# Performance work log

Measured on AMD Instinct MI355X. Metric: run time of the kernel, lower is better.

The kernel has to match this reference:

```python
import jax, jax.numpy as jnp
import numpy as np

N, NFEAT, NHID, NCLASS, NHEADS = 4096, 512, 64, 40, 8
ALPHA = 0.2
NEG = -9e15


def setup_inputs() -> dict:
    key = jax.random.key(0)
    ks = jax.random.split(key, 6)
    x = jax.random.normal(ks[0], (N, NFEAT), dtype=jnp.float32)
    adj = jax.random.randint(ks[1], (2, N, N), 0, 2, dtype=jnp.int32)
    # Xavier-ish scaled params
    W1 = jax.random.normal(ks[2], (NHEADS, NFEAT, NHID), dtype=jnp.float32) * (1.0 / np.sqrt(NFEAT))
    a1 = jax.random.normal(ks[3], (NHEADS, 2, NHID), dtype=jnp.float32) * (1.0 / np.sqrt(2 * NHID))
    Wo = jax.random.normal(ks[4], (NHEADS * NHID, NCLASS), dtype=jnp.float32) * (1.0 / np.sqrt(NHEADS * NHID))
    ao = jax.random.normal(ks[5], (2, NCLASS), dtype=jnp.float32) * (1.0 / np.sqrt(2 * NCLASS))
    return {"x": x, "adj": adj, "W1": W1, "a1": a1, "Wo": Wo, "ao": ao}


def _gat_layer(h, adj_mask, W, a_src, a_dst, concat):
    # h: [N,F]; W: [...,F,F']; a_src/a_dst: [...,F']
    if W.ndim == 3:  # multi-head: [H,F,F']
        Wh = jnp.einsum('nf,hfd->hnd', h, W)              # [H,N,F']
        f1 = jnp.einsum('hnd,hd->hn', Wh, a_src)           # [H,N]
        f2 = jnp.einsum('hnd,hd->hn', Wh, a_dst)
        e = jax.nn.leaky_relu(f1[:, :, None] + f2[:, None, :], ALPHA)  # [H,N,N]
        e = jnp.where(adj_mask[None], e, NEG)
        att = jax.nn.softmax(e, axis=-1)
        out = jnp.einsum('hnm,hmd->hnd', att, Wh)          # [H,N,F']
    else:
        Wh = h @ W                                         # [N,F']
        f1 = Wh @ a_src
        f2 = Wh @ a_dst
        e = jax.nn.leaky_relu(f1[:, None] + f2[None, :], ALPHA)
        e = jnp.where(adj_mask, e, NEG)
        att = jax.nn.softmax(e, axis=-1)
        out = att @ Wh
    return jax.nn.elu(out) if concat else out


def reference(x, adj, W1, a1, Wo, ao):
    adj1 = adj[1] > 0
    adj0 = adj[0] > 0
    # layer 1: NHEADS heads, concat=True
    h = _gat_layer(x, adj1, W1, a1[:, 0], a1[:, 1], concat=True)   # [H,N,NHID]
    h = jnp.transpose(h, (1, 0, 2)).reshape(x.shape[0], -1)        # [N, H*NHID]
    # output layer: concat=False, then outer ELU + log_softmax
    out = _gat_layer(h, adj0, Wo, ao[0], ao[1], concat=False)      # [N, NCLASS]
    out = jax.nn.elu(out)
    return jax.nn.log_softmax(out, axis=1)
```

## Files before the change

### kernel.cpp

```cpp
#include <hip/hip_runtime.h>
#include <hip/hip_bf16.h>

#define N      4096
#define NFEAT  512
#define NHID   64
#define NHEADS 8
#define NCLASS 40
#define ALPHA  0.2f
#define LOG2E  1.44269504f

typedef unsigned short u16;
typedef unsigned int   u32;
typedef __attribute__((ext_vector_type(8))) short bf16x8;
typedef __attribute__((ext_vector_type(4))) float f32x4;

__device__ __forceinline__ float b2f(u16 u) {
    return __uint_as_float(((u32)u) << 16);
}
__device__ __forceinline__ u32 rnd_hi(float f) {
    u32 u = __float_as_uint(f);
    return u + 0x7FFFu + ((u >> 16) & 1u);
}
__device__ __forceinline__ u32 pk2(float lo, float hi) {
    __hip_bfloat162 h = __float22bfloat162_rn(make_float2(lo, hi));
    return *(u32*)&h;
}
__device__ __forceinline__ u16 f2b(float f) {
    return (u16)(rnd_hi(f) >> 16);
}
__device__ __forceinline__ float ex2(float t) {
    return __builtin_amdgcn_exp2f(t);
}
__device__ __forceinline__ bf16x8 ones_frag() {
    union { u16 u[8]; bf16x8 v; } o;
    #pragma unroll
    for (int j = 0; j < 8; ++j) o.u[j] = 0x3F80;
    return o.v;
}

__global__ __launch_bounds__(256) void kcx(const float* __restrict__ x,
                                           u16* __restrict__ xb) {
    const int g = blockIdx.x * 256 + threadIdx.x;
    const size_t base = (size_t)g * 8;
    float4 v0 = *(const float4*)&x[base];
    float4 v1 = *(const float4*)&x[base + 4];
    uint4 o;
    o.x = pk2(v0.x, v0.y); o.y = pk2(v0.z, v0.w);
    o.z = pk2(v1.x, v1.y); o.w = pk2(v1.z, v1.w);
    *(uint4*)&xb[base] = o;
}

__global__ __launch_bounds__(256) void kcw(const float* __restrict__ W1,
                                           u16* __restrict__ W1b) {
    __shared__ float ts[64 * 68];
    const int t  = threadIdx.x;
    const int f0 = blockIdx.x * 64;
    const int h  = blockIdx.y;
    #pragma unroll
    for (int i = 0; i < 4; ++i) {
        int flat = t + 256 * i;
        int row = flat >> 4;
        int c4  = (flat & 15) * 4;
        *(float4*)&ts[row * 68 + c4] =
            *(const float4*)&W1[((size_t)h * 512 + f0 + row) * 64 + c4];
    }
    __syncthreads();
    const int d  = t >> 2;
    const int fs = (t & 3) * 16;
    u32 p[8];
    #pragma unroll
    for (int j = 0; j < 8; ++j)
        p[j] = pk2(ts[(fs + 2 * j) * 68 + d], ts[(fs + 2 * j + 1) * 68 + d]);
    u32* dst = (u32*)&W1b[((size_t)(h * 64 + d)) * 512 + f0 + fs];
    *(uint4*)dst       = make_uint4(p[0], p[1], p[2], p[3]);
    *(uint4*)(dst + 4) = make_uint4(p[4], p[5], p[6], p[7]);
}

__global__ __launch_bounds__(256, 4) void k1m_gemm1(const u16* __restrict__ xb,
                                                    const u16* __restrict__ W1b,
                                                    const float* __restrict__ a1,
                                                    u16* __restrict__ Wh1T,
                                                    float* __restrict__ E1p,
                                                    float* __restrict__ E1n,
                                                    float* __restrict__ E2p,
                                                    float* __restrict__ E2n) {
    __shared__ u16 xs[64 * 72];
    __shared__ u16 wvs[64 * 72];
    const int t    = threadIdx.x;
    const int n0   = blockIdx.x * 64;
    const int h    = blockIdx.y;
    const int lane = t & 63;
    const int l15  = lane & 15;
    const int q    = lane >> 4;
    const int wrow = (t >> 6) * 16;
    f32x4 acc[4];
    #pragma unroll
    for (int df = 0; df < 4; ++df)
        #pragma unroll
        for (int r = 0; r < 4; ++r) acc[df][r] = 0.f;
    for (int f0 = 0; f0 < 512; f0 += 64) {
        uint4 sx[2], sw[2];
        #pragma unroll
        for (int i = 0; i < 2; ++i) {
            int flat = t + 256 * i;
            int row = flat >> 3;
            int c8  = (flat & 7) * 8;
            sx[i] = *(const uint4*)&xb[(size_t)(n0 + row) * 512 + f0 + c8];
            sw[i] = *(const uint4*)&W1b[((size_t)(h * 64 + row)) * 512 + f0 + c8];
        }
        __syncthreads();
        #pragma unroll
        for (int i = 0; i < 2; ++i) {
            int flat = t + 256 * i;
            int row = flat >> 3;
            int c8  = (flat & 7) * 8;
            *(uint4*)&xs[row * 72 + c8]  = sx[i];
            *(uint4*)&wvs[row * 72 + c8] = sw[i];
        }
        __syncthreads();
        #pragma unroll
        for (int ks = 0; ks < 2; ++ks) {
            int k0 = ks * 32 + q * 8;
            bf16x8 a = *(const bf16x8*)&xs[(wrow + l15) * 72 + k0];
            #pragma unroll
            for (int df = 0; df < 4; ++df) {
                bf16x8 b = *(const bf16x8*)&wvs[(df * 16 + l15) * 72 + k0];
                acc[df] = __builtin_amdgcn_mfma_f32_16x16x32_bf16(a, b, acc[df], 0, 0, 0);
            }
        }
    }
    #pragma unroll
    for (int df = 0; df < 4; ++df) {
        uint2 o;
        o.x = pk2(acc[df][0], acc[df][1]);
        o.y = pk2(acc[df][2], acc[df][3]);
        *(uint2*)&Wh1T[((size_t)(h * 64 + df * 16 + l15)) * 4096 + n0 + wrow + q * 4] = o;
    }
    float a1v[4], a2v[4];
    #pragma unroll
    for (int df = 0; df < 4; ++df) {
        a1v[df] = a1[h * 128 + df * 16 + l15];
        a2v[df] = a1[h * 128 + 64 + df * 16 + l15];
    }
    #pragma unroll
    for (int r = 0; r < 4; ++r) {
        float s1 = 0.f, s2 = 0.f;
        #pragma unroll
        for (int df = 0; df < 4; ++df) {
            s1 += acc[df][r] * a1v[df];
            s2 += acc[df][r] * a2v[df];
        }
        #pragma unroll
        for (int off = 8; off >= 1; off >>= 1) {
            s1 += __shfl_xor(s1, off);
            s2 += __shfl_xor(s2, off);
        }
        if (l15 == 0) {
            int n = n0 + wrow + q * 4 + r;
            float z1 = s1 * LOG2E, z2 = s2 * LOG2E;
            E1p[h * 4096 + n] = ex2(z1);
            E1n[h * 4096 + n] = ex2(ALPHA * z1);
            E2p[h * 4096 + n] = ex2(z2);
            E2n[h * 4096 + n] = ex2(ALPHA * z2);
        }
    }
}

__global__ __launch_bounds__(256, 4) void k3_attn1(const int* __restrict__ adj1,
                                                   const u16* __restrict__ Wh1T,
                                                   const float* __restrict__ E1p,
                                                   const float* __restrict__ E1n,
                                                   const float* __restrict__ E2p,
                                                   const float* __restrict__ E2n,
                                                   float* __restrict__ pacc1,
                                                   float* __restrict__ pz1) {
    __shared__ u16  wbf[64 * 136];
    __shared__ u16  whT[64 * 136];
    __shared__ float f1ps[64];
    __shared__ float f1ns[64];
    const int t     = threadIdx.x;
    const int n0    = blockIdx.x * 64;
    const int h     = blockIdx.y;
    const int chunk = blockIdx.z;
    const int lane  = t & 63;
    const int l15   = lane & 15;
    const int q     = lane >> 4;
    const int wrow  = (t >> 6) * 16;
    const int c4    = (t & 31) * 4;
    const int rg    = t >> 5;
    const bf16x8 bones = ones_frag();
    if (t < 64) {
        f1ps[t] = E1p[h * N + n0 + t];
        f1ns[t] = E1n[h * N + n0 + t];
    }
    f32x4 acc[5];
    #pragma unroll
    for (int df = 0; df < 5; ++df)
        #pragma unroll
        for (int r = 0; r < 4; ++r) acc[df][r] = 0.f;

    const int mbeg = chunk * 2048;
    int4 aprev[8];
    #pragma unroll
    for (int i = 0; i < 8; ++i)
        aprev[i] = *(const int4*)&adj1[(size_t)(n0 + rg + 8 * i) * N + mbeg + c4];
    float4 P2 = *(const float4*)&E2p[h * N + mbeg + c4];
    float4 N2 = *(const float4*)&E2n[h * N + mbeg + c4];
    __syncthreads();

    for (int m0 = mbeg; m0 < mbeg + 2048; m0 += 128) {
        #pragma unroll
        for (int i = 0; i < 8; ++i) {
            int rr = rg + 8 * i;
            int4 a4 = aprev[i];
            float cp = f1ps[rr];
            float cn = f1ns[rr];
            float w0 = a4.x ? fmaxf(cp * P2.x, cn * N2.x) : 0.f;
            float w1 = a4.y ? fmaxf(cp * P2.y, cn * N2.y) : 0.f;
            float w2 = a4.z ? fmaxf(cp * P2.z, cn * N2.z) : 0.f;
            float w3 = a4.w ? fmaxf(cp * P2.w, cn * N2.w) : 0.f;
            uint2 pk;
            pk.x = pk2(w0, w1);
            pk.y = pk2(w2, w3);
            *(uint2*)&wbf[rr * 136 + c4] = pk;
        }
        int mn = (m0 + 128 < mbeg + 2048) ? m0 + 128 : mbeg;
        #pragma unroll
        for (int i = 0; i < 8; ++i)
            aprev[i] = *(const int4*)&adj1[(size_t)(n0 + rg + 8 * i) * N + mn + c4];
        P2 = *(const float4*)&E2p[h * N + mn + c4];
        N2 = *(const float4*)&E2n[h * N + mn + c4];
        #pragma unroll
        for (int i = 0; i < 4; ++i) {
            int flat = t + 256 * i;
            int row = flat >> 4;
            int c8  = (flat & 15) * 8;
            *(uint4*)&whT[row * 136 + c8] =
                *(const uint4*)&Wh1T[((size_t)(h * 64 + row)) * 4096 + m0 + c8];
        }
        __syncthreads();
        #pragma unroll
        for (int ks = 0; ks < 4; ++ks) {
            int k0 = ks * 32 + q * 8;
            bf16x8 a = *(const bf16x8*)&wbf[(wrow + l15) * 136 + k0];
            #pragma unroll
            for (int df = 0; df < 4; ++df) {
                bf16x8 b = *(const bf16x8*)&whT[(df * 16 + l15) * 136 + k0];
                acc[df] = __builtin_amdgcn_mfma_f32_16x16x32_bf16(a, b, acc[df], 0, 0, 0);
            }
            acc[4] = __builtin_amdgcn_mfma_f32_16x16x32_bf16(a, bones, acc[4], 0, 0, 0);
        }
        __syncthreads();
    }
    const size_t rowbase = (size_t)(chunk * 8 + h) * 4096 + n0;
    #pragma unroll
    for (int r = 0; r < 4; ++r) {
        int nl = wrow + q * 4 + r;
        if (l15 == 0) pz1[rowbase + nl] = acc[4][r];
        #pragma unroll
        for (int df = 0; df < 4; ++df)
            pacc1[(rowbase + nl) * 64 + df * 16 + l15] = acc[df][r];
    }
}

__global__ __launch_bounds__(256) void k3b_norm(const float* __restrict__ pacc1,
                                                const float* __restrict__ pz1,
                                                float* __restrict__ h1) {
    const int g = blockIdx.x * 256 + threadIdx.x;
    const int d = g & 63;
    const int h = (g >> 6) & 7;
    const int n = g >> 9;
    const size_t i0 = (size_t)h * 4096 + n;
    float s = pacc1[i0 * 64 + d] + pacc1[(i0 + 8 * 4096) * 64 + d];
    float z = pz1[i0] + pz1[i0 + 8 * 4096];
    float v = s / fmaxf(z, 1e-30f);
    h1[(size_t)n * 512 + h * 64 + d] = v > 0.f ? v : __expf(v) - 1.f;
}

__global__ __launch_bounds__(256) void k4_gemm2(const float* __restrict__ h1,
                                                const float* __restrict__ Wo,
                                                const float* __restrict__ ao,
                                                float* __restrict__ E1op,
                                                float* __restrict__ E1on,
                                                float* __restrict__ E2op,
                                                float* __restrict__ E2on,
                                                u16* __restrict__ Wh2T) {
    const int t = threadIdx.x;
    const int c = t & 63;
    const int n = blockIdx.x * 4 + (t >> 6);
    float acc = 0.f;
    if (c < NCLASS) {
        const float* hrow = &h1[(size_t)n * 512];
        #pragma unroll 8
        for (int f = 0; f < 512; ++f)
            acc += hrow[f] * Wo[f * NCLASS + c];
        Wh2T[(size_t)c * 4096 + n] = f2b(acc);
    }
    float s1 = (c < NCLASS) ? acc * ao[c] : 0.f;
    float s2 = (c < NCLASS) ? acc * ao[NCLASS + c] : 0.f;
    #pragma unroll
    for (int off = 32; off >= 1; off >>= 1) {
        s1 += __shfl_xor(s1, off);
        s2 += __shfl_xor(s2, off);
    }
    if (c == 0) {
        float z1 = s1 * LOG2E, z2 = s2 * LOG2E;
        E1op[n] = ex2(z1);
        E1on[n] = ex2(ALPHA * z1);
        E2op[n] = ex2(z2);
        E2on[n] = ex2(ALPHA * z2);
    }
}

__global__ __launch_bounds__(256, 4) void k5a_attn2(const int* __restrict__ adj0,
                                                    const u16* __restrict__ Wh2T,
                                                    const float* __restrict__ E1op,
                                                    const float* __restrict__ E1on,
                                                    const float* __restrict__ E2op,
                                                    const float* __restrict__ E2on,
                                                    float* __restrict__ pacc,
                                                    float* __restrict__ pz) {
    __shared__ u16  wbf[64 * 136];
    __shared__ u16  whT[48 * 136];
    __shared__ float f1ps[64];
    __shared__ float f1ns[64];
    const int t     = threadIdx.x;
    const int n0    = blockIdx.x * 64;
    const int chunk = blockIdx.y;
    const int mbase = chunk * 256;
    const int lane  = t & 63;
    const int l15   = lane & 15;
    const int q     = lane >> 4;
    const int wrow  = (t >> 6) * 16;
    const int c4    = (t & 31) * 4;
    const int rg    = t >> 5;
    const bf16x8 bones = ones_frag();
    if (t < 64) {
        f1ps[t] = E1op[n0 + t];
        f1ns[t] = E1on[n0 + t];
    }
    #pragma unroll
    for (int i = 0; i < 5; ++i) {
        int idx = t + 256 * i;
        if (idx < 1088) whT[40 * 136 + idx] = 0;
    }
    f32x4 acc[4];
    #pragma unroll
    for (int df = 0; df < 4; ++df)
        #pragma unroll
        for (int r = 0; r < 4; ++r) acc[df][r] = 0.f;
    int4 aprev[8];
    #pragma unroll
    for (int i = 0; i < 8; ++i)
        aprev[i] = *(const int4*)&adj0[(size_t)(n0 + rg + 8 * i) * N + mbase + c4];
    float4 P2 = *(const float4*)&E2op[mbase + c4];
    float4 N2 = *(const float4*)&E2on[mbase + c4];
    __syncthreads();

    for (int mt = 0; mt < 2; ++mt) {
        int m0 = mbase + mt * 128;
        #pragma unroll
        for (int i = 0; i < 8; ++i) {
            int rr = rg + 8 * i;
            int4 a4 = aprev[i];
            float cp = f1ps[rr];
            float cn = f1ns[rr];
            float w0 = a4.x ? fmaxf(cp * P2.x, cn * N2.x) : 0.f;
            float w1 = a4.y ? fmaxf(cp * P2.y, cn * N2.y) : 0.f;
            float w2 = a4.z ? fmaxf(cp * P2.z, cn * N2.z) : 0.f;
            float w3 = a4.w ? fmaxf(cp * P2.w, cn * N2.w) : 0.f;
            uint2 pk;
            pk.x = pk2(w0, w1);
            pk.y = pk2(w2, w3);
            *(uint2*)&wbf[rr * 136 + c4] = pk;
        }
        int mn = mbase + ((mt + 1) & 1) * 128;
        #pragma unroll
        for (int i = 0; i < 8; ++i)
            aprev[i] = *(const int4*)&adj0[(size_t)(n0 + rg + 8 * i) * N + mn + c4];
        P2 = *(const float4*)&E2op[mn + c4];
        N2 = *(const float4*)&E2on[mn + c4];
        #pragma unroll
        for (int i = 0; i < 3; ++i) {
            int flat = t + 256 * i;
            if (flat < 640) {
                int row = flat >> 4;
                int c8  = (flat & 15) * 8;
                *(uint4*)&whT[row * 136 + c8] =
                    *(const uint4*)&Wh2T[(size_t)row * 4096 + m0 + c8];
            }
        }
        __syncthreads();
        #pragma unroll
        for (int ks = 0; ks < 4; ++ks) {
            int k0 = ks * 32 + q * 8;
            bf16x8 a = *(const bf16x8*)&wbf[(wrow + l15) * 136 + k0];
            #pragma unroll
            for (int df = 0; df < 3; ++df) {
                bf16x8 b = *(const bf16x8*)&whT[(df * 16 + l15) * 136 + k0];
                acc[df] = __builtin_amdgcn_mfma_f32_16x16x32_bf16(a, b, acc[df], 0, 0, 0);
            }
            acc[3] = __builtin_amdgcn_mfma_f32_16x16x32_bf16(a, bones, acc[3], 0, 0, 0);
        }
        __syncthreads();
    }
    #pragma unroll
    for (int r = 0; r < 4; ++r) {
        int n = n0 + wrow + q * 4 + r;
        if (l15 == 0) pz[(size_t)chunk * N + n] = acc[3][r];
        #pragma unroll
        for (int df = 0; df < 3; ++df) {
            int c = df * 16 + l15;
            if (c < NCLASS)
                pacc[((size_t)chunk * N + n) * NCLASS + c] = acc[df][r];
        }
    }
}

__global__ __launch_bounds__(256) void k5b_final(const float* __restrict__ pacc,
                                                 const float* __restrict__ pz,
                                                 float* __restrict__ out) {
    const int t = threadIdx.x;
    const int lane = t & 63;
    const int n = blockIdx.x * 4 + (t >> 6);
    float s = 0.f, Z = 0.f;
    #pragma unroll
    for (int ch = 0; ch < 16; ++ch) {
        Z += pz[(size_t)ch * N + n];
        if (lane < NCLASS) s += pacc[(size_t)(ch * N + n) * NCLASS + lane];
    }
    float v;
    if (lane < NCLASS) {
        v = s / fmaxf(Z, 1e-30f);
        v = v > 0.f ? v : __expf(v) - 1.f;
    } else {
        v = -INFINITY;
    }
    float mx = v;
    #pragma unroll
    for (int off = 32; off >= 1; off >>= 1) mx = fmaxf(mx, __shfl_xor(mx, off));
    float ex = (lane < NCLASS) ? __expf(v - mx) : 0.f;
    #pragma unroll
    for (int off = 32; off >= 1; off >>= 1) ex += __shfl_xor(ex, off);
    float lse = mx + __logf(ex);
    if (lane < NCLASS) out[(size_t)n * NCLASS + lane] = v - lse;
}

extern "C" void kernel_launch(void* const* d_in, const int* in_sizes, int n_in,
                              void* d_out, int out_size, void* d_ws, size_t ws_size,
                              hipStream_t stream) {
    const float* x   = (const float*)d_in[0];
    const int*   adj = (const int*)d_in[1];
    const float* W1  = (const float*)d_in[2];
    const float* a1  = (const float*)d_in[3];
    const float* Wo  = (const float*)d_in[4];
    const float* ao  = (const float*)d_in[5];

    float* ws    = (float*)d_ws;
    float* h1    = ws;
    float* E1p   = h1 + 2097152;
    float* E1n   = E1p + 32768;
    float* E2p   = E1n + 32768;
    float* E2n   = E2p + 32768;
    float* E1op  = E2n + 32768;
    float* E1on  = E1op + 4096;
    float* E2op  = E1on + 4096;
    float* E2on  = E2op + 4096;
    float* pz    = E2on + 4096;
    float* pz1   = pz + 65536;
    u16*   Wh1T  = (u16*)(pz1 + 65536);
    u16*   Wh2T  = Wh1T + 2097152;
    float* R     = (float*)(Wh2T + 163840);
    u16*   xb    = (u16*)R;
    u16*   W1b   = xb + 2097152;
    float* pacc1 = R;
    float* pacc  = R;

    const int* adj0 = adj;
    const int* adj1 = adj + (size_t)N * N;

    hipLaunchKernelGGL(kcx,       dim3(1024),     dim3(256), 0, stream, x, xb);
    hipLaunchKernelGGL(kcw,       dim3(8, 8),     dim3(256), 0, stream, W1, W1b);
    hipLaunchKernelGGL(k1m_gemm1, dim3(64, 8),    dim3(256), 0, stream, xb, W1b, a1, Wh1T, E1p, E1n, E2p, E2n);
    hipLaunchKernelGGL(k3_attn1,  dim3(64, 8, 2), dim3(256), 0, stream, adj1, Wh1T, E1p, E1n, E2p, E2n, pacc1, pz1);
    hipLaunchKernelGGL(k3b_norm,  dim3(8192),     dim3(256), 0, stream, pacc1, pz1, h1);
    hipLaunchKernelGGL(k4_gemm2,  dim3(1024),     dim3(256), 0, stream, h1, Wo, ao, E1op, E1on, E2op, E2on, Wh2T);
    hipLaunchKernelGGL(k5a_attn2, dim3(64, 16),   dim3(256), 0, stream, adj0, Wh2T, E1op, E1on, E2op, E2on, pacc, pz);
    hipLaunchKernelGGL(k5b_final, dim3(1024),     dim3(256), 0, stream, pacc, pz, (float*)d_out);
}
```

Baseline: 336.0 us.

## Read attention B operand directly from global and double-buffer weight tile

Both attention kernels stop staging the Wh^T tile through shared memory. Each wave now loads its MFMA B fragments straight from global memory through per-lane row pointers. The weight tile in shared memory is double-buffered so the trailing barrier of each iteration can go, and in the second kernel the zero-fill of padding rows is dropped. The goal is less LDS traffic and fewer barriers, at the cost of global-load latency inside the MFMA loop and redundant loads across the four waves. The output-layer kernel may also read rows past the 40 classes of Wh2T.

```diff
diff --git a/kernel.cpp b/kernel.cpp
--- a/kernel.cpp
+++ b/kernel.cpp
@@ -174,8 +174,7 @@
                                                    const float* __restrict__ E2n,
                                                    float* __restrict__ pacc1,
                                                    float* __restrict__ pz1) {
-    __shared__ u16  wbf[64 * 136];
-    __shared__ u16  whT[64 * 136];
+    __shared__ u16  wbf[2][64 * 136];
     __shared__ float f1ps[64];
     __shared__ float f1ns[64];
     const int t     = threadIdx.x;
@@ -193,6 +192,10 @@
         f1ps[t] = E1p[h * N + n0 + t];
         f1ns[t] = E1n[h * N + n0 + t];
     }
+    const u16* Brow[4];
+    #pragma unroll
+    for (int df = 0; df < 4; ++df)
+        Brow[df] = &Wh1T[((size_t)(h * 64 + df * 16 + l15)) * 4096];
     f32x4 acc[5];
     #pragma unroll
     for (int df = 0; df < 5; ++df)
@@ -208,6 +211,7 @@
     float4 N2 = *(const float4*)&E2n[h * N + mbeg + c4];
     __syncthreads();
 
+    int buf = 0;
     for (int m0 = mbeg; m0 < mbeg + 2048; m0 += 128) {
         #pragma unroll
         for (int i = 0; i < 8; ++i) {
@@ -222,7 +226,7 @@
             uint2 pk;
             pk.x = pk2(w0, w1);
             pk.y = pk2(w2, w3);
-            *(uint2*)&wbf[rr * 136 + c4] = pk;
+            *(uint2*)&wbf[buf][rr * 136 + c4] = pk;
         }
         int mn = (m0 + 128 < mbeg + 2048) ? m0 + 128 : mbeg;
         #pragma unroll
@@ -230,27 +234,19 @@
             aprev[i] = *(const int4*)&adj1[(size_t)(n0 + rg + 8 * i) * N + mn + c4];
         P2 = *(const float4*)&E2p[h * N + mn + c4];
         N2 = *(const float4*)&E2n[h * N + mn + c4];
-        #pragma unroll
-        for (int i = 0; i < 4; ++i) {
-            int flat = t + 256 * i;
-            int row = flat >> 4;
-            int c8  = (flat & 15) * 8;
-            *(uint4*)&whT[row * 136 + c8] =
-                *(const uint4*)&Wh1T[((size_t)(h * 64 + row)) * 4096 + m0 + c8];
-        }
         __syncthreads();
         #pragma unroll
         for (int ks = 0; ks < 4; ++ks) {
             int k0 = ks * 32 + q * 8;
-            bf16x8 a = *(const bf16x8*)&wbf[(wrow + l15) * 136 + k0];
+            bf16x8 a = *(const bf16x8*)&wbf[buf][(wrow + l15) * 136 + k0];
             #pragma unroll
             for (int df = 0; df < 4; ++df) {
-                bf16x8 b = *(const bf16x8*)&whT[(df * 16 + l15) * 136 + k0];
+                bf16x8 b = *(const bf16x8*)&Brow[df][m0 + k0];
                 acc[df] = __builtin_amdgcn_mfma_f32_16x16x32_bf16(a, b, acc[df], 0, 0, 0);
             }
             acc[4] = __builtin_amdgcn_mfma_f32_16x16x32_bf16(a, bones, acc[4], 0, 0, 0);
         }
-        __syncthreads();
+        buf ^= 1;
     }
     const size_t rowbase = (size_t)(chunk * 8 + h) * 4096 + n0;
     #pragma unroll
@@ -320,8 +316,7 @@
                                                     const float* __restrict__ E2on,
                                                     float* __restrict__ pacc,
                                                     float* __restrict__ pz) {
-    __shared__ u16  wbf[64 * 136];
-    __shared__ u16  whT[48 * 136];
+    __shared__ u16  wbf[2][64 * 136];
     __shared__ float f1ps[64];
     __shared__ float f1ns[64];
     const int t     = threadIdx.x;
@@ -339,11 +334,10 @@
         f1ps[t] = E1op[n0 + t];
         f1ns[t] = E1on[n0 + t];
     }
-    #pragma unroll
-    for (int i = 0; i < 5; ++i) {
-        int idx = t + 256 * i;
-        if (idx < 1088) whT[40 * 136 + idx] = 0;
-    }
+    const u16* Brow[3];
+    #pragma unroll
+    for (int df = 0; df < 3; ++df)
+        Brow[df] = &Wh2T[((size_t)(df * 16 + l15)) * 4096];
     f32x4 acc[4];
     #pragma unroll
     for (int df = 0; df < 4; ++df)
@@ -357,6 +351,7 @@
     float4 N2 = *(const float4*)&E2on[mbase + c4];
     __syncthreads();
 
+    int buf = 0;
     for (int mt = 0; mt < 2; ++mt) {
         int m0 = mbase + mt * 128;
         #pragma unroll
@@ -372,7 +367,7 @@
             uint2 pk;
             pk.x = pk2(w0, w1);
             pk.y = pk2(w2, w3);
-            *(uint2*)&wbf[rr * 136 + c4] = pk;
+            *(uint2*)&wbf[buf][rr * 136 + c4] = pk;
         }
         int mn = mbase + ((mt + 1) & 1) * 128;
         #pragma unroll
@@ -380,29 +375,19 @@
             aprev[i] = *(const int4*)&adj0[(size_t)(n0 + rg + 8 * i) * N + mn + c4];
         P2 = *(const float4*)&E2op[mn + c4];
         N2 = *(const float4*)&E2on[mn + c4];
-        #pragma unroll
-        for (int i = 0; i < 3; ++i) {
-            int flat = t + 256 * i;
-            if (flat < 640) {
-                int row = flat >> 4;
-                int c8  = (flat & 15) * 8;
-                *(uint4*)&whT[row * 136 + c8] =
-                    *(const uint4*)&Wh2T[(size_t)row * 4096 + m0 + c8];
-            }
-        }
         __syncthreads();
         #pragma unroll
         for (int ks = 0; ks < 4; ++ks) {
             int k0 = ks * 32 + q * 8;
-            bf16x8 a = *(const bf16x8*)&wbf[(wrow + l15) * 136 + k0];
+            bf16x8 a = *(const bf16x8*)&wbf[buf][(wrow + l15) * 136 + k0];
             #pragma unroll
             for (int df = 0; df < 3; ++df) {
-                bf16x8 b = *(const bf16x8*)&whT[(df * 16 + l15) * 136 + k0];
+                bf16x8 b = *(const bf16x8*)&Brow[df][m0 + k0];
                 acc[df] = __builtin_amdgcn_mfma_f32_16x16x32_bf16(a, b, acc[df], 0, 0, 0);
             }
             acc[3] = __builtin_amdgcn_mfma_f32_16x16x32_bf16(a, bones, acc[3], 0, 0, 0);
         }
-        __syncthreads();
+        buf ^= 1;
     }
     #pragma unroll
     for (int r = 0; r < 4; ++r) {
```

Result: slower. 424.6 us (+26.4%).
